# Optimization experiments

Hardware: AMD Instinct MI355X
Metric: run time of the kernel (lower is better)

Reference implementation:

```python
import jax, jax.numpy as jnp
import numpy as np

N = 512      # number of nodes
D = 512      # input_dim
H = 64       # relation-net hidden dim
OUT = 32     # gcn output dim
BN_EPS = 1e-5


def setup_inputs() -> dict:
    key = jax.random.key(0)
    ks = jax.random.split(key, 6)
    features = jax.random.normal(ks[0], (N, D), dtype=jnp.float32)
    # RelationNetwork: Linear(2D, H) + ReLU + Linear(H, 1) + Sigmoid
    rel_w1 = jax.random.normal(ks[1], (2 * D, H), dtype=jnp.float32) * np.float32(1.0 / np.sqrt(2 * D))
    rel_b1 = jnp.zeros((H,), jnp.float32)
    rel_w2 = jax.random.normal(ks[2], (H, 1), dtype=jnp.float32) * np.float32(1.0 / np.sqrt(H))
    rel_b2 = jnp.zeros((1,), jnp.float32)
    # GraphConvolution weight (kaiming fan_in) + bias
    gcn_w = jax.random.normal(ks[3], (D, OUT), dtype=jnp.float32) * np.float32(np.sqrt(2.0 / D))
    gcn_b = jnp.zeros((OUT,), jnp.float32)
    # BatchNorm1d(32) in eval mode: running_mean=0, running_var=1
    bn_gamma = jnp.ones((OUT,), jnp.float32)
    bn_beta = jnp.zeros((OUT,), jnp.float32)
    return {"features": features, "rel_w1": rel_w1, "rel_b1": rel_b1,
            "rel_w2": rel_w2, "rel_b2": rel_b2, "gcn_w": gcn_w, "gcn_b": gcn_b,
            "bn_gamma": bn_gamma, "bn_beta": bn_beta}


def reference(features, rel_w1, rel_b1, rel_w2, rel_b2, gcn_w, gcn_b, bn_gamma, bn_beta):
    n, d = features.shape
    # temp1 = features.repeat(N,1)        -> row (i*N+j) = features[j]
    # temp2 = features.repeat(1,N).view   -> row (i*N+j) = features[i]
    # temp  = cat([temp1, temp2], dim=1)  -> pair[i,j] = [features[j], features[i]]
    fj = jnp.broadcast_to(features[None, :, :], (n, n, d))
    fi = jnp.broadcast_to(features[:, None, :], (n, n, d))
    pair = jnp.concatenate([fj, fi], axis=-1)               # (N, N, 2D) -- dominant intermediate
    h = jax.nn.relu(jnp.einsum('ijk,kh->ijh', pair, rel_w1) + rel_b1)
    adj = jax.nn.sigmoid(jnp.einsum('ijh,ho->ijo', h, rel_w2)[..., 0] + rel_b2[0])  # (N, N)
    A = jnp.eye(n, dtype=features.dtype) + adj
    # D = diag(sqrt(rowsum + 1)); inv(D) A inv(D) == A / (d_i * d_j)
    dvec = jnp.sqrt(jnp.sum(A, axis=1) + 1.0)
    A = A / (dvec[:, None] * dvec[None, :])
    # GraphConvolution: A @ X @ W + b
    x = A @ (features @ gcn_w) + gcn_b                      # (N, 32)
    # BatchNorm1d(32), eval mode (running_mean=0, running_var=1), then ReLU; dropout is a no-op in eval
    x = bn_gamma * x * jnp.float32(1.0 / np.sqrt(1.0 + BN_EPS)) + bn_beta
    x = jax.nn.relu(x)
    return (x, A)
```

## Files before the change

kernel.cpp:

```cpp
#include <hip/hip_runtime.h>
#include <math.h>

#define NN 512
#define DD 512
#define HH 64
#define OUTC 32


template<int STRIDE>
__device__ __forceinline__ void dotrows(const float* __restrict__ fp,
                                        const float* __restrict__ wp,
                                        float4 acc[4])
{
    float4 fr[4][4];
    #pragma unroll
    for (int r = 0; r < 4; ++r)
        #pragma unroll
        for (int q = 0; q < 4; ++q)
            fr[r][q] = *(const float4*)(fp + (size_t)r * DD + 4 * q);

    #pragma unroll
    for (int q = 0; q < 16; ++q) {
        float4 w = *(const float4*)(wp + (size_t)q * STRIDE);
        #pragma unroll
        for (int r = 0; r < 4; ++r) {
            float f = (q < 4 ? (q == 0 ? fr[r][0].x : q == 1 ? fr[r][0].y : q == 2 ? fr[r][0].z : fr[r][0].w)
                     : q < 8 ? (q == 4 ? fr[r][1].x : q == 5 ? fr[r][1].y : q == 6 ? fr[r][1].z : fr[r][1].w)
                     : q < 12 ? (q == 8 ? fr[r][2].x : q == 9 ? fr[r][2].y : q == 10 ? fr[r][2].z : fr[r][2].w)
                     : (q == 12 ? fr[r][3].x : q == 13 ? fr[r][3].y : q == 14 ? fr[r][3].z : fr[r][3].w));
            acc[r].x = fmaf(f, w.x, acc[r].x);
            acc[r].y = fmaf(f, w.y, acc[r].y);
            acc[r].z = fmaf(f, w.z, acc[r].z);
            acc[r].w = fmaf(f, w.w, acc[r].w);
        }
    }
}

__global__ __launch_bounds__(256) void k1_gemm(
    const float* __restrict__ features,
    const float* __restrict__ rel_w1,
    const float* __restrict__ rel_b1,
    const float* __restrict__ gcn_w,
    float* __restrict__ p1t,
    float* __restrict__ p2b,
    float* __restrict__ xw)
{
    __shared__ float sred[4][32][33];
    const int t  = threadIdx.x;
    const int tq = t & 7;
    const int kc = t >> 3;
    const int cg = blockIdx.x;
    const int i0 = blockIdx.y * 4;

    const float* fp = features + (size_t)i0 * DD + kc * 16;

    float4 acc[4];
    #pragma unroll
    for (int r = 0; r < 4; ++r) acc[r] = make_float4(0.f, 0.f, 0.f, 0.f);

    if (cg < 2)
        dotrows<HH>(fp, rel_w1 + cg * 32 + tq * 4 + (size_t)kc * 16 * HH, acc);
    else if (cg < 4)
        dotrows<HH>(fp, rel_w1 + (size_t)DD * HH + (cg - 2) * 32 + tq * 4
                        + (size_t)kc * 16 * HH, acc);
    else
        dotrows<OUTC>(fp, gcn_w + tq * 4 + (size_t)kc * 16 * OUTC, acc);

    #pragma unroll
    for (int r = 0; r < 4; ++r) {
        sred[r][kc][tq * 4 + 0] = acc[r].x;
        sred[r][kc][tq * 4 + 1] = acc[r].y;
        sred[r][kc][tq * 4 + 2] = acc[r].z;
        sred[r][kc][tq * 4 + 3] = acc[r].w;
    }
    __syncthreads();

    if (t < 128) {
        const int r = t >> 5, c = t & 31;
        const int i = i0 + r;
        float s = 0.f;
        #pragma unroll
        for (int k = 0; k < 32; ++k) s += sred[r][k][c];
        if (cg < 2) {
            p1t[(size_t)(cg * 32 + c) * NN + i] = s;
        } else if (cg < 4) {
            int h = (cg - 2) * 32 + c;
            p2b[(size_t)i * HH + h] = s + rel_b1[h];
        } else {
            xw[(size_t)i * OUTC + c] = s;
        }
    }
}

__global__ __launch_bounds__(512) void k2_adj(
    const float* __restrict__ p1t,
    const float* __restrict__ p2b,
    const float* __restrict__ rel_w2,
    const float* __restrict__ rel_b2,
    float* __restrict__ araw,
    float* __restrict__ rdv)
{
    __shared__ float sred[2][8];
    const int t  = threadIdx.x;
    const int i0 = blockIdx.x * 2;

    const float* p20 = p2b + (size_t)i0 * HH;
    const float* p21 = p20 + HH;

    float a0 = rel_b2[0], a1 = a0;
    #pragma unroll
    for (int k = 0; k < HH; ++k) {
        float pv = p1t[(size_t)k * NN + t];
        float w  = rel_w2[k];
        a0 = fmaf(fmaxf(pv + p20[k], 0.f), w, a0);
        a1 = fmaf(fmaxf(pv + p21[k], 0.f), w, a1);
    }
    a0 = 1.f / (1.f + expf(-a0));
    a1 = 1.f / (1.f + expf(-a1));
    if (t == i0)     a0 += 1.f;
    if (t == i0 + 1) a1 += 1.f;
    araw[(size_t)i0 * NN + t]       = a0;
    araw[(size_t)(i0 + 1) * NN + t] = a1;

    float rs0 = a0, rs1 = a1;
    #pragma unroll
    for (int off = 32; off > 0; off >>= 1) {
        rs0 += __shfl_down(rs0, off, 64);
        rs1 += __shfl_down(rs1, off, 64);
    }
    const int wv = t >> 6, ln = t & 63;
    if (ln == 0) { sred[0][wv] = rs0; sred[1][wv] = rs1; }
    __syncthreads();
    if (t < 2) {
        float s = 0.f;
        #pragma unroll
        for (int w = 0; w < 8; ++w) s += sred[t][w];
        rdv[i0 + t] = 1.0f / sqrtf(s + 1.0f);
    }
}

__global__ __launch_bounds__(512) void k3_gcn(
    const float* __restrict__ xw,
    const float* __restrict__ rdv,
    const float* __restrict__ gcn_b,
    const float* __restrict__ bn_gamma,
    const float* __restrict__ bn_beta,
    float* __restrict__ outx,
    float* __restrict__ outA)
{
    __shared__ float sdv[NN];
    __shared__ float sA[2][NN];
    __shared__ float sredC[2][16][33];
    const int t  = threadIdx.x;
    const int i0 = blockIdx.x * 2;

    sdv[t] = rdv[t];
    __syncthreads();

    const float dj  = sdv[t];
    const float an0 = outA[(size_t)i0 * NN + t]       * (sdv[i0] * dj);
    const float an1 = outA[(size_t)(i0 + 1) * NN + t] * (sdv[i0 + 1] * dj);
    outA[(size_t)i0 * NN + t]       = an0;
    outA[(size_t)(i0 + 1) * NN + t] = an1;
    sA[0][t] = an0;
    sA[1][t] = an1;
    __syncthreads();

    const int o  = t & 31;
    const int ch = t >> 5;
    float acc0 = 0.f, acc1 = 0.f;
    #pragma unroll
    for (int jj = 0; jj < 32; ++jj) {
        int j = ch * 32 + jj;
        float xv = xw[(size_t)j * OUTC + o];
        acc0 = fmaf(sA[0][j], xv, acc0);
        acc1 = fmaf(sA[1][j], xv, acc1);
    }
    sredC[0][ch][o] = acc0;
    sredC[1][ch][o] = acc1;
    __syncthreads();

    if (t < 64) {
        const int rr = t >> 5, oc = t & 31;
        float v = gcn_b[oc];
        #pragma unroll
        for (int c = 0; c < 16; ++c) v += sredC[rr][c][oc];
        const float invs = 1.0f / sqrtf(1.0f + 1e-5f);
        v = bn_gamma[oc] * v * invs + bn_beta[oc];
        outx[(size_t)(i0 + rr) * OUTC + oc] = fmaxf(v, 0.f);
    }
}

extern "C" void kernel_launch(void* const* d_in, const int* in_sizes, int n_in,
                              void* d_out, int out_size, void* d_ws, size_t ws_size,
                              hipStream_t stream) {
    const float* features = (const float*)d_in[0];
    const float* rel_w1   = (const float*)d_in[1];
    const float* rel_b1   = (const float*)d_in[2];
    const float* rel_w2   = (const float*)d_in[3];
    const float* rel_b2   = (const float*)d_in[4];
    const float* gcn_w    = (const float*)d_in[5];
    const float* gcn_b    = (const float*)d_in[6];
    const float* bn_gamma = (const float*)d_in[7];
    const float* bn_beta  = (const float*)d_in[8];

    float* out  = (float*)d_out;
    float* outx = out;
    float* outA = out + NN * OUTC;

    float* ws  = (float*)d_ws;
    float* p1t = ws;
    float* p2b = ws + 32768;
    float* xw  = ws + 65536;
    float* rdv = ws + 81920;

    hipLaunchKernelGGL(k1_gemm, dim3(5, 128), dim3(256), 0, stream,
                       features, rel_w1, rel_b1, gcn_w, p1t, p2b, xw);
    hipLaunchKernelGGL(k2_adj, dim3(256), dim3(512), 0, stream,
                       p1t, p2b, rel_w2, rel_b2, outA, rdv);
    hipLaunchKernelGGL(k3_gcn, dim3(256), dim3(512), 0, stream,
                       xw, rdv, gcn_b, bn_gamma, bn_beta, outx, outA);
}
```

Before: 17.92 us.

## Process 8 rows per k1 block and pack p1 in float4-interleaved layout

k1 now computes 8 feature rows per block instead of 4, so each weight float4 load is reused across twice as many rows and the grid shrinks to 64 row-groups. It also stores the p1 projection as groups of 4 hidden units interleaved per node, which lets k2 read it with float4 loads instead of scalar strided loads. The cost is higher register and shared-memory use in k1 (larger sred) and fewer blocks to spread over the CUs.

```diff
diff --git a/kernel.cpp b/kernel.cpp
--- a/kernel.cpp
+++ b/kernel.cpp
@@ -41,33 +41,39 @@
     const float* __restrict__ rel_w1,
     const float* __restrict__ rel_b1,
     const float* __restrict__ gcn_w,
-    float* __restrict__ p1t,
+    float* __restrict__ p1p,
     float* __restrict__ p2b,
     float* __restrict__ xw)
 {
-    __shared__ float sred[4][32][33];
+    __shared__ float sred[8][32][33];
     const int t  = threadIdx.x;
     const int tq = t & 7;
     const int kc = t >> 3;
     const int cg = blockIdx.x;
-    const int i0 = blockIdx.y * 4;
+    const int i0 = blockIdx.y * 8;
 
     const float* fp = features + (size_t)i0 * DD + kc * 16;
 
-    float4 acc[4];
-    #pragma unroll
-    for (int r = 0; r < 4; ++r) acc[r] = make_float4(0.f, 0.f, 0.f, 0.f);
-
-    if (cg < 2)
-        dotrows<HH>(fp, rel_w1 + cg * 32 + tq * 4 + (size_t)kc * 16 * HH, acc);
-    else if (cg < 4)
-        dotrows<HH>(fp, rel_w1 + (size_t)DD * HH + (cg - 2) * 32 + tq * 4
-                        + (size_t)kc * 16 * HH, acc);
-    else
-        dotrows<OUTC>(fp, gcn_w + tq * 4 + (size_t)kc * 16 * OUTC, acc);
-
-    #pragma unroll
-    for (int r = 0; r < 4; ++r) {
+    float4 acc[8];
+    #pragma unroll
+    for (int r = 0; r < 8; ++r) acc[r] = make_float4(0.f, 0.f, 0.f, 0.f);
+
+    const float* wp;
+    if (cg < 2)      wp = rel_w1 + cg * 32 + tq * 4 + (size_t)kc * 16 * HH;
+    else if (cg < 4) wp = rel_w1 + (size_t)DD * HH + (cg - 2) * 32 + tq * 4
+                          + (size_t)kc * 16 * HH;
+    else             wp = gcn_w + tq * 4 + (size_t)kc * 16 * OUTC;
+
+    if (cg < 4) {
+        dotrows<HH>(fp, wp, acc);
+        dotrows<HH>(fp + 4 * DD, wp, acc + 4);
+    } else {
+        dotrows<OUTC>(fp, wp, acc);
+        dotrows<OUTC>(fp + 4 * DD, wp, acc + 4);
+    }
+
+    #pragma unroll
+    for (int r = 0; r < 8; ++r) {
         sred[r][kc][tq * 4 + 0] = acc[r].x;
         sred[r][kc][tq * 4 + 1] = acc[r].y;
         sred[r][kc][tq * 4 + 2] = acc[r].z;
@@ -75,16 +81,17 @@
     }
     __syncthreads();
 
-    if (t < 128) {
+    {
         const int r = t >> 5, c = t & 31;
         const int i = i0 + r;
         float s = 0.f;
         #pragma unroll
         for (int k = 0; k < 32; ++k) s += sred[r][k][c];
         if (cg < 2) {
-            p1t[(size_t)(cg * 32 + c) * NN + i] = s;
+            const int h = cg * 32 + c;
+            p1p[(size_t)(h >> 2) * (NN * 4) + (size_t)i * 4 + (h & 3)] = s;
         } else if (cg < 4) {
-            int h = (cg - 2) * 32 + c;
+            const int h = (cg - 2) * 32 + c;
             p2b[(size_t)i * HH + h] = s + rel_b1[h];
         } else {
             xw[(size_t)i * OUTC + c] = s;
@@ -93,7 +100,7 @@
 }
 
 __global__ __launch_bounds__(512) void k2_adj(
-    const float* __restrict__ p1t,
+    const float* __restrict__ p1p,
     const float* __restrict__ p2b,
     const float* __restrict__ rel_w2,
     const float* __restrict__ rel_b2,
@@ -109,11 +116,19 @@
 
     float a0 = rel_b2[0], a1 = a0;
     #pragma unroll
-    for (int k = 0; k < HH; ++k) {
-        float pv = p1t[(size_t)k * NN + t];
-        float w  = rel_w2[k];
-        a0 = fmaf(fmaxf(pv + p20[k], 0.f), w, a0);
-        a1 = fmaf(fmaxf(pv + p21[k], 0.f), w, a1);
+    for (int k4 = 0; k4 < 16; ++k4) {
+        float4 pv = *(const float4*)(p1p + (size_t)k4 * (NN * 4) + (size_t)t * 4);
+        const int kb = 4 * k4;
+        float w0 = rel_w2[kb + 0], w1 = rel_w2[kb + 1];
+        float w2 = rel_w2[kb + 2], w3 = rel_w2[kb + 3];
+        a0 = fmaf(fmaxf(pv.x + p20[kb + 0], 0.f), w0, a0);
+        a1 = fmaf(fmaxf(pv.x + p21[kb + 0], 0.f), w0, a1);
+        a0 = fmaf(fmaxf(pv.y + p20[kb + 1], 0.f), w1, a0);
+        a1 = fmaf(fmaxf(pv.y + p21[kb + 1], 0.f), w1, a1);
+        a0 = fmaf(fmaxf(pv.z + p20[kb + 2], 0.f), w2, a0);
+        a1 = fmaf(fmaxf(pv.z + p21[kb + 2], 0.f), w2, a1);
+        a0 = fmaf(fmaxf(pv.w + p20[kb + 3], 0.f), w3, a0);
+        a1 = fmaf(fmaxf(pv.w + p21[kb + 3], 0.f), w3, a1);
     }
     a0 = 1.f / (1.f + expf(-a0));
     a1 = 1.f / (1.f + expf(-a1));
@@ -209,15 +224,15 @@
     float* outA = out + NN * OUTC;
 
     float* ws  = (float*)d_ws;
-    float* p1t = ws;
+    float* p1p = ws;
     float* p2b = ws + 32768;
     float* xw  = ws + 65536;
     float* rdv = ws + 81920;
 
-    hipLaunchKernelGGL(k1_gemm, dim3(5, 128), dim3(256), 0, stream,
-                       features, rel_w1, rel_b1, gcn_w, p1t, p2b, xw);
+    hipLaunchKernelGGL(k1_gemm, dim3(5, 64), dim3(256), 0, stream,
+                       features, rel_w1, rel_b1, gcn_w, p1p, p2b, xw);
     hipLaunchKernelGGL(k2_adj, dim3(256), dim3(512), 0, stream,
-                       p1t, p2b, rel_w2, rel_b2, outA, rdv);
+                       p1p, p2b, rel_w2, rel_b2, outA, rdv);
     hipLaunchKernelGGL(k3_gcn, dim3(256), dim3(512), 0, stream,
                        xw, rdv, gcn_b, bn_gamma, bn_beta, outx, outA);
 }
```

Result: no change. 17.65 us (-1.5%).
